# Kernel optimization log

Hardware: AMD Instinct MI355X
Metric: run time of the kernel (lower is better)

The kernel has to match this reference:

```python
import jax, jax.numpy as jnp
import numpy as np

ANCHORS_ALL = jnp.array([[10.,13.],[16.,30.],[33.,23.],[30.,61.],[62.,45.],
                         [59.,119.],[116.,90.],[156.,198.],[373.,326.]], dtype=jnp.float32)
INDICES = jnp.array([0, 1, 2], dtype=jnp.int32)   # anchor indices of level 0
ANCH_LVL = ANCHORS_ALL[0:3]                        # [nA, 2] anchors for this level
STRIDE = 8.0
N_CLS = 80
NA = 3


def _bce_logits(x, t):
    # elementwise binary_cross_entropy_with_logits (same formula as torch)
    return jnp.maximum(x, 0.0) - x * t + jnp.log1p(jnp.exp(-jnp.abs(x)))


def _iou_cxcywh(a, b):
    # a: [..., 4], b: [..., 4] (broadcastable), boxes as (cx, cy, w, h)
    ax1, ax2 = a[..., 0] - a[..., 2] * 0.5, a[..., 0] + a[..., 2] * 0.5
    ay1, ay2 = a[..., 1] - a[..., 3] * 0.5, a[..., 1] + a[..., 3] * 0.5
    bx1, bx2 = b[..., 0] - b[..., 2] * 0.5, b[..., 0] + b[..., 2] * 0.5
    by1, by2 = b[..., 1] - b[..., 3] * 0.5, b[..., 1] + b[..., 3] * 0.5
    iw = jnp.clip(jnp.minimum(ax2, bx2) - jnp.maximum(ax1, bx1), 0.0)
    ih = jnp.clip(jnp.minimum(ay2, by2) - jnp.maximum(ay1, by1), 0.0)
    inter = iw * ih
    union = (ax2 - ax1) * (ay2 - ay1) + (bx2 - bx1) * (by2 - by1) - inter
    return inter / (union + 1e-16)


def setup_inputs() -> dict:
    key = jax.random.key(0)
    ks = jax.random.split(key, 7)
    nB, nA, nH, nW, G = 8, 3, 160, 160, 32
    t_bbox = jax.random.normal(ks[0], (nB, nA, nH, nW, 4), jnp.float32)
    conf_logits = jax.random.normal(ks[1], (nB, nA, nH, nW, 1), jnp.float32)
    cls_logits = jax.random.normal(ks[2], (nB, nA, nH, nW, N_CLS), jnp.float32)
    cxy = jax.random.uniform(ks[3], (nB, G, 2), jnp.float32, 20.0, 1260.0)
    wh = jax.random.uniform(ks[4], (nB, G, 2), jnp.float32, 5.0, 60.0)
    gt_bboxes = jnp.concatenate([cxy, wh], axis=-1)           # cxcywh
    gt_cls = jax.random.randint(ks[5], (nB, G), 0, N_CLS, jnp.int32)
    gt_mask = jax.random.uniform(ks[6], (nB, G)) < 0.8        # padded-GT validity
    return dict(t_bbox=t_bbox, conf_logits=conf_logits, cls_logits=cls_logits,
                gt_bboxes=gt_bboxes, gt_cls=gt_cls, gt_mask=gt_mask)


def reference(t_bbox, conf_logits, cls_logits, gt_bboxes, gt_cls, gt_mask):
    nB, nA, nH, nW, _ = t_bbox.shape
    N = nA * nH * nW
    # ---- bbox decode (torch does this on a detached copy) ----
    sig = jax.nn.sigmoid(jax.lax.stop_gradient(t_bbox))
    yv, xv = jnp.meshgrid(jnp.arange(nH), jnp.arange(nW), indexing='ij')
    grid = jnp.stack([xv, yv], axis=-1).astype(jnp.float32).reshape(1, 1, nH, nW, 2)
    p_xy = (sig[..., 0:2] * 2.0 - 0.5 + grid) * STRIDE
    p_wh = (sig[..., 2:4] * 2.0) ** 2 * ANCH_LVL.reshape(1, nA, 1, 1, 2)
    p_bbox = jnp.concatenate([p_xy, p_wh], axis=-1).reshape(nB, N, 4)
    p_conf = jax.nn.sigmoid(jax.lax.stop_gradient(conf_logits))       # [nB,nA,nH,nW,1]
    p_cls = jax.nn.sigmoid(jax.lax.stop_gradient(cls_logits))
    cls_score = jnp.max(p_cls, axis=-1, keepdims=True)
    cls_idx = jnp.argmax(p_cls, axis=-1).reshape(nB, N)
    score = (p_conf * cls_score).reshape(nB, N)
    # ---- per-GT best-anchor matching (vectorized over [nB, G]) ----
    gw, gh = gt_bboxes[..., 2], gt_bboxes[..., 3]
    aw, ah = ANCHORS_ALL[:, 0], ANCHORS_ALL[:, 1]
    inter = jnp.minimum(gw[..., None], aw) * jnp.minimum(gh[..., None], ah)
    union = (gw * gh)[..., None] + aw * ah - inter
    anch_idx = jnp.argmax(inter / (union + 1e-16), axis=-1)           # [nB,G]
    matched = jnp.any(anch_idx[..., None] == INDICES, axis=-1)
    valid = gt_mask & matched
    ta = (anch_idx % NA).astype(jnp.int32)
    ti = jnp.clip((gt_bboxes[..., 0] / STRIDE).astype(jnp.int32), 0, nW - 1)
    tj = jnp.clip((gt_bboxes[..., 1] / STRIDE).astype(jnp.int32), 0, nH - 1)
    b_idx = jnp.arange(nB)[:, None]
    t_bb = t_bbox[b_idx, ta, tj, ti]       # [nB,G,4]
    t_cl = cls_logits[b_idx, ta, tj, ti]   # [nB,G,C]
    tgt_xy = ((gt_bboxes[..., 0:2] / STRIDE) % 1.0 + 0.5) / 2.0
    tgt_wh = jnp.sqrt(gt_bboxes[..., 2:4] / ANCH_LVL[ta]) / 2.0
    vm = valid.astype(t_bbox.dtype)
    loss_xy = jnp.sum(vm * jnp.sum(_bce_logits(t_bb[..., 0:2], tgt_xy), axis=-1))
    loss_wh = jnp.sum(vm * jnp.sum(_bce_logits(t_bb[..., 2:4], tgt_wh), axis=-1))
    onehot = jax.nn.one_hot(gt_cls, N_CLS, dtype=t_bbox.dtype)
    loss_cls = jnp.sum(vm * jnp.mean(_bce_logits(t_cl, onehot), axis=-1))
    # ---- objectness target: max IoU of every decoded box with the GTs ----
    ious = _iou_cxcywh(p_bbox[:, :, None, :], gt_bboxes[:, None, :, :])  # [nB,N,G]
    ious = jnp.where(gt_mask[:, None, :], ious, -1.0)
    has_gt = jnp.any(gt_mask, axis=-1)
    tconf = jnp.where(has_gt[:, None], jnp.max(ious, axis=-1), 0.0)
    tconf = tconf.reshape(nB, nA, nH, nW, 1)
    loss_conf = jnp.sum(_bce_logits(conf_logits, tconf))
    loss = (loss_xy + loss_wh + loss_conf + loss_cls) / nB
    return p_bbox, cls_idx, score, loss
```

## Files before the change

### kernel.cpp

```cpp
#include <hip/hip_runtime.h>

#define NB 8
#define NA 3
#define NH 160
#define NW 160
#define NCLS 80
#define NGT 32
#define NPB (NA * NH * NW)
#define TOTAL (NB * NPB)
#define OFF_CLSIDX (TOTAL * 4)
#define OFF_SCORE  (TOTAL * 5)
#define OFF_LOSS   (TOTAL * 6)

#define F4_PER_ROW 20
#define LDS_ROW_F4 21

__device__ float g_acc;

__device__ __forceinline__ float det_sigmoid(float x) { return 1.0f / (1.0f + expf(-x)); }
__device__ __forceinline__ float det_bce(float x, float t) {
    return fmaxf(x, 0.0f) - x * t + log1pf(expf(-fabsf(x)));
}
__device__ __forceinline__ float det_aw3(int a) { return a == 0 ? 10.0f : (a == 1 ? 16.0f : 33.0f); }
__device__ __forceinline__ float det_ah3(int a) { return a == 0 ? 13.0f : (a == 1 ? 30.0f : 23.0f); }

__device__ __forceinline__ bool det_mask_is_u8(const void* p) {
    const unsigned int* w = (const unsigned int*)p;
    unsigned int acc = 0;
#pragma unroll
    for (int k = 0; k < 64; k++) acc |= (w[k] & 0xFFFFFF00u);
    return acc != 0;
}
__device__ __forceinline__ bool det_mask_at(const void* p, bool u8mode, int idx) {
    return u8mode ? (((const unsigned char*)p)[idx] != 0)
                  : (((const int*)p)[idx] != 0);
}

__global__ void det_zero_k() { g_acc = 0.0f; }

__global__ void det_gt_k(const float* __restrict__ t_bbox,
                         const float* __restrict__ cls_logits,
                         const float* __restrict__ gt_bboxes,
                         const int* __restrict__ gt_cls,
                         const void* __restrict__ gt_mask) {
    __shared__ int s_u8;
    if (threadIdx.x == 0) s_u8 = det_mask_is_u8(gt_mask) ? 1 : 0;
    __syncthreads();
    bool u8mode = (s_u8 != 0);

    int t = threadIdx.x;
    int b = t >> 5;
    int g = t & 31;
    float4 gtb = ((const float4*)gt_bboxes)[b * NGT + g];
    float cx = gtb.x, cy = gtb.y, gw = gtb.z, gh = gtb.w;

    const float aw9[9] = {10.f,16.f,33.f,30.f,62.f,59.f,116.f,156.f,373.f};
    const float ah9[9] = {13.f,30.f,23.f,61.f,45.f,119.f,90.f,198.f,326.f};
    float garea = gw * gh;
    int aidx = 0;
    float best = -1.0f;
#pragma unroll
    for (int k = 0; k < 9; k++) {
        float inter = fminf(gw, aw9[k]) * fminf(gh, ah9[k]);
        float uni = garea + aw9[k] * ah9[k] - inter;
        float r = inter / (uni + 1e-16f);
        if (r > best) { best = r; aidx = k; }
    }
    bool valid = det_mask_at(gt_mask, u8mode, b * NGT + g) && (aidx < NA);
    int ta = aidx % NA;
    int ti = min(max((int)(cx * 0.125f), 0), NW - 1);
    int tj = min(max((int)(cy * 0.125f), 0), NH - 1);
    size_t cell = ((size_t)(b * NA + ta) * NH + tj) * NW + ti;

    float4 tb = ((const float4*)t_bbox)[cell];
    float fx = cx * 0.125f; fx -= floorf(fx);
    float fy = cy * 0.125f; fy -= floorf(fy);
    float tx = (fx + 0.5f) * 0.5f;
    float ty = (fy + 0.5f) * 0.5f;
    float tw = sqrtf(gw / det_aw3(ta)) * 0.5f;
    float th = sqrtf(gh / det_ah3(ta)) * 0.5f;

    float l = det_bce(tb.x, tx) + det_bce(tb.y, ty) +
              det_bce(tb.z, tw) + det_bce(tb.w, th);

    const float4* cl = (const float4*)(cls_logits + cell * NCLS);
    int tc = gt_cls[b * NGT + g];
    float lc = 0.0f;
#pragma unroll
    for (int c4 = 0; c4 < NCLS / 4; c4++) {
        float4 v = cl[c4];
        int c = c4 * 4;
        lc += det_bce(v.x, (c + 0 == tc) ? 1.0f : 0.0f);
        lc += det_bce(v.y, (c + 1 == tc) ? 1.0f : 0.0f);
        lc += det_bce(v.z, (c + 2 == tc) ? 1.0f : 0.0f);
        lc += det_bce(v.w, (c + 3 == tc) ? 1.0f : 0.0f);
    }
    l += lc * (1.0f / NCLS);
    if (valid) atomicAdd(&g_acc, l);
}

__global__ __launch_bounds__(256) void det_main_k(
    const float* __restrict__ t_bbox,
    const float* __restrict__ conf_logits,
    const float* __restrict__ cls_logits,
    const float* __restrict__ gt_bboxes,
    const void* __restrict__ gt_mask,
    float* __restrict__ out) {
    __shared__ float4 s_cls[4][16 * LDS_ROW_F4];
    __shared__ float s_x1[NGT], s_y1[NGT], s_x2[NGT], s_y2[NGT], s_ar[NGT];
    __shared__ float s_m[NGT];
    __shared__ float s_part[4];
    __shared__ int s_u8;

    int tid = threadIdx.x;
    int blockCell = blockIdx.x * 256;
    int gid = blockCell + tid;
    int b = gid / NPB;
    int r = gid % NPB;

    if (tid == 0) s_u8 = det_mask_is_u8(gt_mask) ? 1 : 0;
    __syncthreads();
    if (tid < NGT) {
        int g = tid;
        float4 gtb = ((const float4*)gt_bboxes)[b * NGT + g];
        s_x1[g] = gtb.x - gtb.z * 0.5f;
        s_x2[g] = gtb.x + gtb.z * 0.5f;
        s_y1[g] = gtb.y - gtb.w * 0.5f;
        s_y2[g] = gtb.y + gtb.w * 0.5f;
        s_ar[g] = gtb.z * gtb.w;
        s_m[g]  = det_mask_at(gt_mask, s_u8 != 0, b * NGT + g) ? 1.0f : 0.0f;
    }
    __syncthreads();

    int a   = r / (NH * NW);
    int rem = r % (NH * NW);
    int j   = rem / NW;
    int i   = rem % NW;

    float4 tb = ((const float4*)t_bbox)[gid];
    float s0 = det_sigmoid(tb.x), s1 = det_sigmoid(tb.y);
    float s2 = det_sigmoid(tb.z), s3 = det_sigmoid(tb.w);
    float px = (s0 * 2.0f - 0.5f + (float)i) * 8.0f;
    float py = (s1 * 2.0f - 0.5f + (float)j) * 8.0f;
    float sw = s2 * 2.0f, sh = s3 * 2.0f;
    float pw = sw * sw * det_aw3(a);
    float ph = sh * sh * det_ah3(a);
    float4 pb; pb.x = px; pb.y = py; pb.z = pw; pb.w = ph;
    ((float4*)out)[gid] = pb;

    float px1 = px - pw * 0.5f, px2 = px + pw * 0.5f;
    float py1 = py - ph * 0.5f, py2 = py + ph * 0.5f;
    float parea = pw * ph;
    float maxiou = 0.0f;
#pragma unroll
    for (int g = 0; g < NGT; g++) {
        float iw = fmaxf(fminf(px2, s_x2[g]) - fmaxf(px1, s_x1[g]), 0.0f);
        float ih = fmaxf(fminf(py2, s_y2[g]) - fmaxf(py1, s_y1[g]), 0.0f);
        float inter = iw * ih;
        float uni = parea + s_ar[g] - inter;
        float iou = inter / (uni + 1e-16f);
        maxiou = fmaxf(maxiou, (s_m[g] != 0.0f) ? iou : 0.0f);
    }

    float confl = conf_logits[gid];
    float sconf = det_sigmoid(confl);
    float lconf = det_bce(confl, maxiou);
#pragma unroll
    for (int off = 32; off > 0; off >>= 1) lconf += __shfl_down(lconf, off, 64);
    int w = tid >> 6, l = tid & 63;
    if (l == 0) s_part[w] = lconf;
    __syncthreads();
    if (tid == 0)
        atomicAdd(&g_acc, s_part[0] + s_part[1] + s_part[2] + s_part[3]);

    int cl_ = l >> 2;
    int q   = l & 3;
    const float4* g4 = (const float4*)cls_logits;
    int wbase = blockCell + w * 64;

#pragma unroll
    for (int it = 0; it < 4; ++it) {
        int tileCell = wbase + it * 16;
        size_t f4base = (size_t)tileCell * F4_PER_ROW;
        __syncthreads();
#pragma unroll
        for (int k = 0; k < 5; ++k) {
            int f = k * 64 + l;
            float4 v = g4[f4base + f];
            int rr = f / F4_PER_ROW;
            int cc = f - rr * F4_PER_ROW;
            s_cls[w][rr * LDS_ROW_F4 + cc] = v;
        }
        __syncthreads();

        float mx = -1e30f;
        int mi = 0;
#pragma unroll
        for (int k = 0; k < 5; ++k) {
            int col = q * 5 + k;
            float4 v = s_cls[w][cl_ * LDS_ROW_F4 + col];
            int c = col * 4;
            if (v.x > mx) { mx = v.x; mi = c + 0; }
            if (v.y > mx) { mx = v.y; mi = c + 1; }
            if (v.z > mx) { mx = v.z; mi = c + 2; }
            if (v.w > mx) { mx = v.w; mi = c + 3; }
        }
#pragma unroll
        for (int s = 1; s < 4; s <<= 1) {
            float ov = __shfl_xor(mx, s, 64);
            int   oi = __shfl_xor(mi, s, 64);
            if (ov > mx || (ov == mx && oi < mi)) { mx = ov; mi = oi; }
        }
        float sc = __shfl(sconf, it * 16 + cl_, 64);
        if (q == 0) {
            int cellg = tileCell + cl_;
            out[OFF_CLSIDX + cellg] = (float)mi;
            out[OFF_SCORE  + cellg] = sc * det_sigmoid(mx);
        }
    }
}

__global__ void det_fin_k(float* __restrict__ out) {
    out[OFF_LOSS] = g_acc * (1.0f / NB);
}

extern "C" void kernel_launch(void* const* d_in, const int* in_sizes, int n_in,
                              void* d_out, int out_size, void* d_ws, size_t ws_size,
                              hipStream_t stream) {
    (void)in_sizes; (void)n_in; (void)out_size; (void)d_ws; (void)ws_size;
    const float* t_bbox      = (const float*)d_in[0];
    const float* conf_logits = (const float*)d_in[1];
    const float* cls_logits  = (const float*)d_in[2];
    const float* gt_bboxes   = (const float*)d_in[3];
    const int*   gt_cls      = (const int*)d_in[4];
    const void*  gt_mask     = (const void*)d_in[5];
    float* out = (float*)d_out;

    det_zero_k<<<1, 1, 0, stream>>>();
    det_gt_k<<<1, 256, 0, stream>>>(t_bbox, cls_logits, gt_bboxes, gt_cls, gt_mask);
    det_main_k<<<TOTAL / 256, 256, 0, stream>>>(t_bbox, conf_logits, cls_logits,
                                                gt_bboxes, gt_mask, out);
    det_fin_k<<<1, 1, 0, stream>>>(out);
}
```

Measured before the change: 329.6 us.

## Replace global atomic loss with workspace partials and prefetch class logits in registers

Result: no change. 331.8 us (+0.7%).

```diff
diff --git a/kernel.cpp b/kernel.cpp
--- a/kernel.cpp
+++ b/kernel.cpp
@@ -13,9 +13,9 @@
 #define OFF_LOSS   (TOTAL * 6)
 
 #define F4_PER_ROW 20
-#define LDS_ROW_F4 21
-
-__device__ float g_acc;
+#define NWAVES (TOTAL / 64)
+#define WS_GT  NWAVES
+#define WS_COUNT (NWAVES + 4)
 
 __device__ __forceinline__ float det_sigmoid(float x) { return 1.0f / (1.0f + expf(-x)); }
 __device__ __forceinline__ float det_bce(float x, float t) {
@@ -35,14 +35,13 @@
     return u8mode ? (((const unsigned char*)p)[idx] != 0)
                   : (((const int*)p)[idx] != 0);
 }
-
-__global__ void det_zero_k() { g_acc = 0.0f; }
 
 __global__ void det_gt_k(const float* __restrict__ t_bbox,
                          const float* __restrict__ cls_logits,
                          const float* __restrict__ gt_bboxes,
                          const int* __restrict__ gt_cls,
-                         const void* __restrict__ gt_mask) {
+                         const void* __restrict__ gt_mask,
+                         float* __restrict__ ws) {
     __shared__ int s_u8;
     if (threadIdx.x == 0) s_u8 = det_mask_is_u8(gt_mask) ? 1 : 0;
     __syncthreads();
@@ -96,7 +95,11 @@
         lc += det_bce(v.w, (c + 3 == tc) ? 1.0f : 0.0f);
     }
     l += lc * (1.0f / NCLS);
-    if (valid) atomicAdd(&g_acc, l);
+
+    float lv = valid ? l : 0.0f;
+#pragma unroll
+    for (int off = 32; off > 0; off >>= 1) lv += __shfl_down(lv, off, 64);
+    if ((t & 63) == 0) ws[WS_GT + (t >> 6)] = lv;
 }
 
 __global__ __launch_bounds__(256) void det_main_k(
@@ -105,11 +108,11 @@
     const float* __restrict__ cls_logits,
     const float* __restrict__ gt_bboxes,
     const void* __restrict__ gt_mask,
-    float* __restrict__ out) {
-    __shared__ float4 s_cls[4][16 * LDS_ROW_F4];
+    float* __restrict__ out,
+    float* __restrict__ ws) {
+    __shared__ float4 s_cls[4][16 * F4_PER_ROW];
     __shared__ float s_x1[NGT], s_y1[NGT], s_x2[NGT], s_y2[NGT], s_ar[NGT];
     __shared__ float s_m[NGT];
-    __shared__ float s_part[4];
     __shared__ int s_u8;
 
     int tid = threadIdx.x;
@@ -162,43 +165,39 @@
         maxiou = fmaxf(maxiou, (s_m[g] != 0.0f) ? iou : 0.0f);
     }
 
+    int w = tid >> 6, l = tid & 63;
     float confl = conf_logits[gid];
     float sconf = det_sigmoid(confl);
     float lconf = det_bce(confl, maxiou);
 #pragma unroll
     for (int off = 32; off > 0; off >>= 1) lconf += __shfl_down(lconf, off, 64);
-    int w = tid >> 6, l = tid & 63;
-    if (l == 0) s_part[w] = lconf;
-    __syncthreads();
-    if (tid == 0)
-        atomicAdd(&g_acc, s_part[0] + s_part[1] + s_part[2] + s_part[3]);
+    if (l == 0) ws[blockIdx.x * 4 + w] = lconf;
 
     int cl_ = l >> 2;
     int q   = l & 3;
     const float4* g4 = (const float4*)cls_logits;
     int wbase = blockCell + w * 64;
+    size_t base0 = (size_t)wbase * F4_PER_ROW;
+
+    float4 pr[5];
+#pragma unroll
+    for (int k = 0; k < 5; ++k) pr[k] = g4[base0 + k * 64 + l];
 
 #pragma unroll
     for (int it = 0; it < 4; ++it) {
-        int tileCell = wbase + it * 16;
-        size_t f4base = (size_t)tileCell * F4_PER_ROW;
-        __syncthreads();
-#pragma unroll
-        for (int k = 0; k < 5; ++k) {
-            int f = k * 64 + l;
-            float4 v = g4[f4base + f];
-            int rr = f / F4_PER_ROW;
-            int cc = f - rr * F4_PER_ROW;
-            s_cls[w][rr * LDS_ROW_F4 + cc] = v;
-        }
-        __syncthreads();
-
+#pragma unroll
+        for (int k = 0; k < 5; ++k) s_cls[w][k * 64 + l] = pr[k];
+        if (it < 3) {
+            size_t bn = base0 + (size_t)(it + 1) * 320;
+#pragma unroll
+            for (int k = 0; k < 5; ++k) pr[k] = g4[bn + k * 64 + l];
+        }
         float mx = -1e30f;
         int mi = 0;
 #pragma unroll
         for (int k = 0; k < 5; ++k) {
             int col = q * 5 + k;
-            float4 v = s_cls[w][cl_ * LDS_ROW_F4 + col];
+            float4 v = s_cls[w][cl_ * F4_PER_ROW + col];
             int c = col * 4;
             if (v.x > mx) { mx = v.x; mi = c + 0; }
             if (v.y > mx) { mx = v.y; mi = c + 1; }
@@ -213,21 +212,29 @@
         }
         float sc = __shfl(sconf, it * 16 + cl_, 64);
         if (q == 0) {
-            int cellg = tileCell + cl_;
+            int cellg = wbase + it * 16 + cl_;
             out[OFF_CLSIDX + cellg] = (float)mi;
             out[OFF_SCORE  + cellg] = sc * det_sigmoid(mx);
         }
     }
 }
 
-__global__ void det_fin_k(float* __restrict__ out) {
-    out[OFF_LOSS] = g_acc * (1.0f / NB);
+__global__ void det_fin_k(const float* __restrict__ ws, float* __restrict__ out) {
+    __shared__ float sp[4];
+    int t = threadIdx.x;
+    float s = 0.0f;
+    for (int idx = t; idx < WS_COUNT; idx += 256) s += ws[idx];
+#pragma unroll
+    for (int off = 32; off > 0; off >>= 1) s += __shfl_down(s, off, 64);
+    if ((t & 63) == 0) sp[t >> 6] = s;
+    __syncthreads();
+    if (t == 0) out[OFF_LOSS] = (sp[0] + sp[1] + sp[2] + sp[3]) * (1.0f / NB);
 }
 
 extern "C" void kernel_launch(void* const* d_in, const int* in_sizes, int n_in,
                               void* d_out, int out_size, void* d_ws, size_t ws_size,
                               hipStream_t stream) {
-    (void)in_sizes; (void)n_in; (void)out_size; (void)d_ws; (void)ws_size;
+    (void)in_sizes; (void)n_in; (void)out_size; (void)ws_size;
     const float* t_bbox      = (const float*)d_in[0];
     const float* conf_logits = (const float*)d_in[1];
     const float* cls_logits  = (const float*)d_in[2];
@@ -235,10 +242,11 @@
     const int*   gt_cls      = (const int*)d_in[4];
     const void*  gt_mask     = (const void*)d_in[5];
     float* out = (float*)d_out;
-
-    det_zero_k<<<1, 1, 0, stream>>>();
-    det_gt_k<<<1, 256, 0, stream>>>(t_bbox, cls_logits, gt_bboxes, gt_cls, gt_mask);
+    float* ws  = (float*)d_ws;
+
+    det_gt_k<<<1, 256, 0, stream>>>(t_bbox, cls_logits, gt_bboxes,
+                                    gt_cls, gt_mask, ws);
     det_main_k<<<TOTAL / 256, 256, 0, stream>>>(t_bbox, conf_logits, cls_logits,
-                                                gt_bboxes, gt_mask, out);
-    det_fin_k<<<1, 1, 0, stream>>>(out);
-}
+                                                gt_bboxes, gt_mask, out, ws);
+    det_fin_k<<<1, 256, 0, stream>>>(ws, out);
+}
```
